# Kernel tuning notes

Hardware: AMD Instinct MI355X
Metric: run time of the kernel (lower is better)

## Reference

```python
import jax, jax.numpy as jnp
import numpy as np
from jax import lax

DIM = 256
MOTION = 128
HEADS = 8
HID = int(DIM * 3.0)
EPS = 1e-5


def std_ln(x, w, b):
    # standard nn.LayerNorm: biased var, /sqrt(var+eps)
    mean = x.mean(-1, keepdims=True)
    var = jnp.var(x, axis=-1, keepdims=True)
    return w * (x - mean) / jnp.sqrt(var + EPS) + b


def custom_ln(x, w, b):
    # repo's custom LayerNorm: UNBIASED std (ddof=1) and divide by (std+eps)
    mean = x.mean(-1, keepdims=True)
    std = jnp.std(x, axis=-1, ddof=1, keepdims=True)
    return w * (x - mean) / (std + EPS) + b


def setup_inputs() -> dict:
    key = jax.random.key(0)
    ks = jax.random.split(key, 32)
    s = 0.02
    d = {}
    d['x'] = jax.random.normal(ks[0], (4, 16384, DIM), jnp.float32)
    d['cor'] = jax.random.uniform(ks[1], (4, 128, 128, 2), jnp.float32)
    # attention projections (qkv_bias=False)
    d['q_w'] = jax.random.normal(ks[2], (DIM, DIM), jnp.float32) * s
    d['kv_w'] = jax.random.normal(ks[3], (2 * DIM, DIM), jnp.float32) * s
    d['cor_w'] = jax.random.normal(ks[4], (MOTION, 2), jnp.float32) * s
    hd = DIM // HEADS
    md = MOTION // HEADS
    d['kln_w'] = jnp.ones((HEADS, 1, hd), jnp.float32)
    d['kln_b'] = jnp.zeros((HEADS, 1, hd), jnp.float32)
    d['vln_w'] = jnp.ones((HEADS, 1, hd), jnp.float32)
    d['vln_b'] = jnp.zeros((HEADS, 1, hd), jnp.float32)
    d['corln_w'] = jnp.ones((HEADS, 1, md), jnp.float32)
    d['corln_b'] = jnp.zeros((HEADS, 1, md), jnp.float32)
    d['op1_w'] = jax.random.normal(ks[5], (DIM, DIM), jnp.float32) * s
    d['op1_b'] = jnp.zeros((DIM,), jnp.float32)
    d['op2_w'] = jax.random.normal(ks[6], (DIM, DIM), jnp.float32) * s
    d['op2_b'] = jnp.zeros((DIM,), jnp.float32)
    d['om1_w'] = jax.random.normal(ks[7], (MOTION, MOTION), jnp.float32) * s
    d['om1_b'] = jnp.zeros((MOTION,), jnp.float32)
    d['om2_w'] = jax.random.normal(ks[8], (MOTION, MOTION), jnp.float32) * s
    d['om2_b'] = jnp.zeros((MOTION,), jnp.float32)
    d['norm1_w'] = jnp.ones((DIM,), jnp.float32)
    d['norm1_b'] = jnp.zeros((DIM,), jnp.float32)
    d['norm2_w'] = jnp.ones((DIM,), jnp.float32)
    d['norm2_b'] = jnp.zeros((DIM,), jnp.float32)
    d['fc1_w'] = jax.random.normal(ks[9], (HID, DIM), jnp.float32) * s
    d['fc1_b'] = jnp.zeros((HID,), jnp.float32)
    d['dw_w'] = jax.random.normal(ks[10], (HID, 1, 3, 3), jnp.float32) * np.sqrt(2.0 / 9.0)
    d['dw_b'] = jnp.zeros((HID,), jnp.float32)
    d['fc2_w'] = jax.random.normal(ks[11], (DIM, HID), jnp.float32) * s
    d['fc2_b'] = jnp.zeros((DIM,), jnp.float32)
    d['H'] = 128
    d['W'] = 128
    d['B'] = 2
    return d


def _forward(x, cor, q_w, kv_w, cor_w, kln_w, kln_b, vln_w, vln_b,
             corln_w, corln_b, op1_w, op1_b, op2_w, op2_b,
             om1_w, om1_b, om2_w, om2_b, norm1_w, norm1_b,
             norm2_w, norm2_b, fc1_w, fc1_b, dw_w, dw_b, fc2_w, fc2_b,
             H, W, B):
    gelu = lambda t: jax.nn.gelu(t, approximate=False)
    nwB = 2 * B
    N = H * W
    C = x.shape[-1]
    M = cor_w.shape[0]
    h = kln_w.shape[0]
    hd = C // h
    md = M // h
    hid = fc1_w.shape[0]

    xw = x.reshape(nwB, N, C)            # window_partition with full window == identity
    corw = cor.reshape(nwB, N, 2)

    xn = std_ln(xw, norm1_w, norm1_b)
    half = nwB // 2
    xr = jnp.concatenate([xn[half:], xn[:half]], axis=0)  # swap frame halves

    q = (xn @ q_w.T).reshape(nwB, N, h, hd).transpose(0, 2, 1, 3)          # bhnd
    kv = (xr @ kv_w.T).reshape(nwB, N, 2, h, hd)
    k = kv[:, :, 0].transpose(0, 2, 1, 3)
    v = kv[:, :, 1].transpose(0, 2, 1, 3)
    ce_flat = corw @ cor_w.T                                               # (nwB,N,M)
    ce = ce_flat.reshape(nwB, N, h, md).transpose(0, 2, 1, 3)

    k = custom_ln(k, kln_w, kln_b)
    v = custom_ln(v, vln_w, vln_b)
    ce = custom_ln(ce, corln_w, corln_b)

    # linear attention: (k^T v)/N then q @ .
    ktv = jnp.einsum('bhnd,bhne->bhde', k, v) / N
    app = jnp.einsum('bhnd,bhde->bhne', q, ktv).transpose(0, 2, 1, 3).reshape(nwB, N, C)
    t = app + xn                                   # shortcut bias = x_norm
    x_app = gelu(t @ op1_w.T + op1_b) @ op2_w.T + op2_b + xn

    ktc = jnp.einsum('bhnd,bhne->bhde', k, ce) / N
    crev = jnp.einsum('bhnd,bhde->bhne', q, ktc).transpose(0, 2, 1, 3).reshape(nwB, N, M)
    dm = crev - ce_flat
    motion = gelu(dm @ om1_w.T + om1_b) @ om2_w.T + om2_b

    x_back = xn + x_app

    # Mlp with depthwise conv
    y = std_ln(x_back, norm2_w, norm2_b)
    h1 = y @ fc1_w.T + fc1_b                       # (nwB,N,hid)
    img = h1.transpose(0, 2, 1).reshape(nwB, hid, H, W)
    conv = lax.conv_general_dilated(img, dw_w, (1, 1), 'SAME',
                                    feature_group_count=hid,
                                    dimension_numbers=('NCHW', 'OIHW', 'NCHW'))
    conv = conv + dw_b[None, :, None, None]
    h2 = gelu(conv.reshape(nwB, hid, N).transpose(0, 2, 1))
    out = h2 @ fc2_w.T + fc2_b

    x_out = xw + out
    return x_out, motion


def reference(x, cor, q_w, kv_w, cor_w, kln_w, kln_b, vln_w, vln_b,
              corln_w, corln_b, op1_w, op1_b, op2_w, op2_b,
              om1_w, om1_b, om2_w, om2_b, norm1_w, norm1_b,
              norm2_w, norm2_b, fc1_w, fc1_b, dw_w, dw_b, fc2_w, fc2_b,
              H, W, B):
    return _forward(x, cor, q_w, kv_w, cor_w, kln_w, kln_b, vln_w, vln_b,
                    corln_w, corln_b, op1_w, op1_b, op2_w, op2_b,
                    om1_w, om1_b, om2_w, om2_b, norm1_w, norm1_b,
                    norm2_w, norm2_b, fc1_w, fc1_b, dw_w, dw_b, fc2_w, fc2_b,
                    H, W, B)
```

## Files before the change

kernel.cpp:

```cpp
#include <hip/hip_runtime.h>
#include <hip/hip_bf16.h>

#define NTOK 65536

typedef __attribute__((ext_vector_type(4))) float f32x4;
typedef __attribute__((ext_vector_type(8))) short bf16x8;

__device__ __forceinline__ float gelu_f(float x){
    float z = -2.30234438f * fmaf(0.044715f * x * x, x, x);
    float e = exp2f(z);
    return x * __builtin_amdgcn_rcpf(1.0f + e);
}
__device__ __forceinline__ float bf2f(unsigned short u){
    union { unsigned int i; float f; } w; w.i = ((unsigned int)u) << 16; return w.f;
}
__device__ __forceinline__ unsigned short f2bf(float f){
    __hip_bfloat16 h = __float2bfloat16(f);
    return *reinterpret_cast<unsigned short*>(&h);
}

__global__ __launch_bounds__(256) void wconv_kernel(const float* __restrict__ q_w, const float* __restrict__ kv_w,
                                                    const float* __restrict__ op1_w, const float* __restrict__ op2_w,
                                                    const float* __restrict__ om1_w, const float* __restrict__ om2_w,
                                                    const float* __restrict__ fc1_w, const float* __restrict__ fc2_w,
                                                    unsigned short* __restrict__ Wb){
    size_t e = ((size_t)blockIdx.x * 256 + threadIdx.x) * 4;
    if (e >= 753664) return;
    const float* src; size_t off;
    if      (e <  65536){ src = q_w;   off = 0; }
    else if (e < 196608){ src = kv_w;  off = 65536; }
    else if (e < 262144){ src = op1_w; off = 196608; }
    else if (e < 327680){ src = op2_w; off = 262144; }
    else if (e < 344064){ src = om1_w; off = 327680; }
    else if (e < 360448){ src = om2_w; off = 344064; }
    else if (e < 557056){ src = fc1_w; off = 360448; }
    else                { src = fc2_w; off = 557056; }
    float4 v = *reinterpret_cast<const float4*>(src + (e - off));
    ushort4 o; o.x = f2bf(v.x); o.y = f2bf(v.y); o.z = f2bf(v.z); o.w = f2bf(v.w);
    *reinterpret_cast<ushort4*>(Wb + e) = o;
}

template<bool BF16IN>
__global__ __launch_bounds__(256) void stdln_kernel(const void* __restrict__ Xp,
                                                    const float* __restrict__ w,
                                                    const float* __restrict__ b,
                                                    unsigned short* __restrict__ out){
    int wv = threadIdx.x >> 6, lane = threadIdx.x & 63;
    int tok0 = (blockIdx.x * 4 + wv) * 8;
    int c0 = lane * 4;
    float4 w4 = *reinterpret_cast<const float4*>(w + c0);
    float4 b4 = *reinterpret_cast<const float4*>(b + c0);
    #pragma unroll 2
    for (int j = 0; j < 8; j++){
        size_t base = (size_t)(tok0 + j) * 256 + c0;
        float v[4];
        if constexpr (BF16IN){
            ushort4 u = *reinterpret_cast<const ushort4*>((const unsigned short*)Xp + base);
            v[0] = bf2f(u.x); v[1] = bf2f(u.y); v[2] = bf2f(u.z); v[3] = bf2f(u.w);
        } else {
            float4 f = *reinterpret_cast<const float4*>((const float*)Xp + base);
            v[0] = f.x; v[1] = f.y; v[2] = f.z; v[3] = f.w;
        }
        float s = v[0] + v[1] + v[2] + v[3];
        #pragma unroll
        for (int m = 1; m < 64; m <<= 1) s += __shfl_xor(s, m, 64);
        float mean = s * (1.0f / 256.0f);
        float ss = 0;
        #pragma unroll
        for (int k = 0; k < 4; k++){ v[k] -= mean; ss = fmaf(v[k], v[k], ss); }
        #pragma unroll
        for (int m = 1; m < 64; m <<= 1) ss += __shfl_xor(ss, m, 64);
        float inv = rsqrtf(ss * (1.0f / 256.0f) + 1e-5f);
        ushort4 o;
        o.x = f2bf(w4.x * v[0] * inv + b4.x);
        o.y = f2bf(w4.y * v[1] * inv + b4.y);
        o.z = f2bf(w4.z * v[2] * inv + b4.z);
        o.w = f2bf(w4.w * v[3] * inv + b4.w);
        *reinterpret_cast<ushort4*>(out + base) = o;
    }
}

__global__ __launch_bounds__(256) void ce_kernel(const float* __restrict__ cor,
                                                 const float* __restrict__ cor_w,
                                                 unsigned short* __restrict__ CEF){
    int m = threadIdx.x & 127, half = threadIdx.x >> 7;
    float w0 = cor_w[m * 2 + 0], w1 = cor_w[m * 2 + 1];
    #pragma unroll 4
    for (int it = 0; it < 16; it++){
        int tok = blockIdx.x * 32 + it * 2 + half;
        float c0 = cor[(size_t)tok * 2 + 0];
        float c1 = cor[(size_t)tok * 2 + 1];
        CEF[(size_t)tok * 128 + m] = f2bf(c0 * w0 + c1 * w1);
    }
}

__global__ __launch_bounds__(256) void ktvc_kernel(const unsigned short* __restrict__ Kb,
                                                   const unsigned short* __restrict__ Vb,
                                                   const unsigned short* __restrict__ CEF,
                                                   const float* __restrict__ kw, const float* __restrict__ kbb,
                                                   const float* __restrict__ vw, const float* __restrict__ vbb,
                                                   const float* __restrict__ cw, const float* __restrict__ cbb,
                                                   float* __restrict__ KTV, float* __restrict__ KTC){
    int bh = blockIdx.x, b = bh >> 3, h = bh & 7;
    __shared__ float Ks[64][33];
    __shared__ float Vs[64][33];
    __shared__ float Cs[64][17];
    int t = threadIdx.x;
    int lr = t >> 2, lq = t & 3;
    int d0 = (t >> 4) * 2, e0 = (t & 15) * 2, e1 = t & 15;
    float kwr[8], kbr[8], vwr[8], vbr[8], cwr[4], cbr[4];
    #pragma unroll
    for (int j = 0; j < 8; j++){
        kwr[j] = kw[h * 32 + lq * 8 + j]; kbr[j] = kbb[h * 32 + lq * 8 + j];
        vwr[j] = vw[h * 32 + lq * 8 + j]; vbr[j] = vbb[h * 32 + lq * 8 + j];
    }
    #pragma unroll
    for (int j = 0; j < 4; j++){
        cwr[j] = cw[h * 16 + lq * 4 + j]; cbr[j] = cbb[h * 16 + lq * 4 + j];
    }
    float a00 = 0, a01 = 0, a10 = 0, a11 = 0;
    float c0a = 0, c1a = 0;
    size_t base = ((size_t)b << 14) + (size_t)blockIdx.y * 1024;
    for (int n0 = 0; n0 < 1024; n0 += 64){
        size_t rowi = base + n0 + lr;
        const ushort4* kp = reinterpret_cast<const ushort4*>(Kb + rowi * 256 + h * 32 + lq * 8);
        ushort4 ka = kp[0], kc = kp[1];
        const ushort4* vp = reinterpret_cast<const ushort4*>(Vb + rowi * 256 + h * 32 + lq * 8);
        ushort4 va = vp[0], vc = vp[1];
        ushort4 ca = *reinterpret_cast<const ushort4*>(CEF + rowi * 128 + h * 16 + lq * 4);
        float kvv[8] = { bf2f(ka.x), bf2f(ka.y), bf2f(ka.z), bf2f(ka.w),
                         bf2f(kc.x), bf2f(kc.y), bf2f(kc.z), bf2f(kc.w) };
        float vvv[8] = { bf2f(va.x), bf2f(va.y), bf2f(va.z), bf2f(va.w),
                         bf2f(vc.x), bf2f(vc.y), bf2f(vc.z), bf2f(vc.w) };
        float cvv[4] = { bf2f(ca.x), bf2f(ca.y), bf2f(ca.z), bf2f(ca.w) };
        float s = 0;
        #pragma unroll
        for (int j = 0; j < 8; j++) s += kvv[j];
        s += __shfl_xor(s, 1, 64); s += __shfl_xor(s, 2, 64);
        float mean = s * (1.0f / 32.0f);
        float ss = 0;
        #pragma unroll
        for (int j = 0; j < 8; j++){ kvv[j] -= mean; ss = fmaf(kvv[j], kvv[j], ss); }
        ss += __shfl_xor(ss, 1, 64); ss += __shfl_xor(ss, 2, 64);
        float inv = 1.0f / (sqrtf(ss * (1.0f / 31.0f)) + 1e-5f);
        #pragma unroll
        for (int j = 0; j < 8; j++) kvv[j] = fmaf(kwr[j] * kvv[j], inv, kbr[j]);
        s = 0;
        #pragma unroll
        for (int j = 0; j < 8; j++) s += vvv[j];
        s += __shfl_xor(s, 1, 64); s += __shfl_xor(s, 2, 64);
        mean = s * (1.0f / 32.0f);
        ss = 0;
        #pragma unroll
        for (int j = 0; j < 8; j++){ vvv[j] -= mean; ss = fmaf(vvv[j], vvv[j], ss); }
        ss += __shfl_xor(ss, 1, 64); ss += __shfl_xor(ss, 2, 64);
        inv = 1.0f / (sqrtf(ss * (1.0f / 31.0f)) + 1e-5f);
        #pragma unroll
        for (int j = 0; j < 8; j++) vvv[j] = fmaf(vwr[j] * vvv[j], inv, vbr[j]);
        s = 0;
        #pragma unroll
        for (int j = 0; j < 4; j++) s += cvv[j];
        s += __shfl_xor(s, 1, 64); s += __shfl_xor(s, 2, 64);
        mean = s * (1.0f / 16.0f);
        ss = 0;
        #pragma unroll
        for (int j = 0; j < 4; j++){ cvv[j] -= mean; ss = fmaf(cvv[j], cvv[j], ss); }
        ss += __shfl_xor(ss, 1, 64); ss += __shfl_xor(ss, 2, 64);
        inv = 1.0f / (sqrtf(ss * (1.0f / 15.0f)) + 1e-5f);
        #pragma unroll
        for (int j = 0; j < 4; j++) cvv[j] = fmaf(cwr[j] * cvv[j], inv, cbr[j]);
        __syncthreads();
        #pragma unroll
        for (int j = 0; j < 8; j++){ Ks[lr][lq * 8 + j] = kvv[j]; Vs[lr][lq * 8 + j] = vvv[j]; }
        #pragma unroll
        for (int j = 0; j < 4; j++) Cs[lr][lq * 4 + j] = cvv[j];
        __syncthreads();
        #pragma unroll 4
        for (int n = 0; n < 64; n++){
            float k0 = Ks[n][d0], k1 = Ks[n][d0 + 1];
            float v0 = Vs[n][e0], v1 = Vs[n][e0 + 1];
            float ce = Cs[n][e1];
            a00 = fmaf(k0, v0, a00); a01 = fmaf(k0, v1, a01);
            a10 = fmaf(k1, v0, a10); a11 = fmaf(k1, v1, a11);
            c0a = fmaf(k0, ce, c0a); c1a = fmaf(k1, ce, c1a);
        }
    }
    const float sc = 1.0f / 16384.0f;
    float* o = KTV + (size_t)bh * 1024;
    atomicAdd(&o[(d0 + 0) * 32 + e0 + 0], a00 * sc);
    atomicAdd(&o[(d0 + 0) * 32 + e0 + 1], a01 * sc);
    atomicAdd(&o[(d0 + 1) * 32 + e0 + 0], a10 * sc);
    atomicAdd(&o[(d0 + 1) * 32 + e0 + 1], a11 * sc);
    float* o2 = KTC + (size_t)bh * 512;
    atomicAdd(&o2[(d0 + 0) * 16 + e1], c0a * sc);
    atomicAdd(&o2[(d0 + 1) * 16 + e1], c1a * sc);
}

__global__ __launch_bounds__(256) void wcomb_kernel(const float* __restrict__ q_w,
                                                    const float* __restrict__ KTV,
                                                    const float* __restrict__ KTC,
                                                    unsigned short* __restrict__ WTC){
    int c = blockIdx.x;
    int b = blockIdx.y;
    int i = threadIdx.x;
    __shared__ float coef[32];
    int h = (c < 256) ? (c >> 5) : ((c - 256) >> 4);
    if (i < 32){
        if (c < 256) coef[i] = KTV[(size_t)((b * 8 + h) << 10) + i * 32 + (c & 31)];
        else         coef[i] = KTC[(size_t)((b * 8 + h) << 9)  + i * 16 + ((c - 256) & 15)];
    }
    __syncthreads();
    float acc = 0;
    #pragma unroll
    for (int d = 0; d < 32; d++) acc = fmaf(q_w[(size_t)(h * 32 + d) * 256 + i], coef[d], acc);
    WTC[((size_t)b * 384 + c) * 256 + i] = f2bf(acc);
}

__global__ __launch_bounds__(192) void dwconv_kernel(const unsigned short* __restrict__ H1,
                                                     const float* __restrict__ dww,
                                                     const float* __restrict__ dwb,
                                                     unsigned short* __restrict__ H2){
    int blk = blockIdx.x;
    int xq = blk & 3;
    int yb = (blk >> 2) & 31;
    int bb = blk >> 7;
    int y0 = yb * 4, x0 = xq * 32;
    int ch = threadIdx.x * 4;
    float w[9][4];
    #pragma unroll
    for (int k = 0; k < 9; k++)
        #pragma unroll
        for (int j = 0; j < 4; j++) w[k][j] = dww[(ch + j) * 9 + k];
    float bias[4] = { dwb[ch], dwb[ch+1], dwb[ch+2], dwb[ch+3] };
    size_t rb[6]; bool rv[6];
    #pragma unroll
    for (int r = 0; r < 6; r++){
        int yr = y0 - 1 + r;
        rv[r] = ((unsigned)yr <= 127u);
        int yc = yr < 0 ? 0 : (yr > 127 ? 127 : yr);
        rb[r] = ((size_t)((bb << 14) + (yc << 7))) * 768 + ch;
    }
    size_t ob[4];
    #pragma unroll
    for (int j = 0; j < 4; j++) ob[j] = ((size_t)((bb << 14) + ((y0 + j) << 7))) * 768 + ch;

    ushort4 cA[6], cB[6], cC[6], cD[6];
    const ushort4 Z = {0, 0, 0, 0};
    #define LOADR(DST, XX) do {                                               \
        int _x = (XX);                                                        \
        bool xv = ((unsigned)_x <= 127u);                                     \
        _Pragma("unroll")                                                     \
        for (int r = 0; r < 6; r++)                                           \
            DST[r] = (xv && rv[r]) ? *reinterpret_cast<const ushort4*>(H1 + rb[r] + (size_t)_x * 768) : Z; \
    } while (0)

    #define EMITB(SA, SB, SC, XX) do {                                        \
        _Pragma("unroll")                                                     \
        for (int j = 0; j < 4; j++){                                          \
            float acc[4];                                                     \
            _Pragma("unroll")                                                 \
            for (int q = 0; q < 4; q++) acc[q] = bias[q];                     \
            _Pragma("unroll")                                                 \
            for (int rr2 = 0; rr2 < 3; rr2++){                                \
                int ri = j + rr2;                                             \
                float a0=bf2f(SA[ri].x),a1=bf2f(SA[ri].y),a2=bf2f(SA[ri].z),a3=bf2f(SA[ri].w); \
                float b0=bf2f(SB[ri].x),b1=bf2f(SB[ri].y),b2=bf2f(SB[ri].z),b3=bf2f(SB[ri].w); \
                float c0=bf2f(SC[ri].x),c1=bf2f(SC[ri].y),c2=bf2f(SC[ri].z),c3=bf2f(SC[ri].w); \
                acc[0]=fmaf(a0,w[rr2*3+0][0],acc[0]); acc[0]=fmaf(b0,w[rr2*3+1][0],acc[0]); acc[0]=fmaf(c0,w[rr2*3+2][0],acc[0]); \
                acc[1]=fmaf(a1,w[rr2*3+0][1],acc[1]); acc[1]=fmaf(b1,w[rr2*3+1][1],acc[1]); acc[1]=fmaf(c1,w[rr2*3+2][1],acc[1]); \
                acc[2]=fmaf(a2,w[rr2*3+0][2],acc[2]); acc[2]=fmaf(b2,w[rr2*3+1][2],acc[2]); acc[2]=fmaf(c2,w[rr2*3+2][2],acc[2]); \
                acc[3]=fmaf(a3,w[rr2*3+0][3],acc[3]); acc[3]=fmaf(b3,w[rr2*3+1][3],acc[3]); acc[3]=fmaf(c3,w[rr2*3+2][3],acc[3]); \
            }                                                                 \
            ushort4 o;                                                        \
            o.x = f2bf(gelu_f(acc[0])); o.y = f2bf(gelu_f(acc[1]));           \
            o.z = f2bf(gelu_f(acc[2])); o.w = f2bf(gelu_f(acc[3]));           \
            *reinterpret_cast<ushort4*>(H2 + ob[j] + (size_t)(XX) * 768) = o; \
        }                                                                     \
    } while (0)

    LOADR(cD, x0 - 1);
    LOADR(cA, x0);
    LOADR(cB, x0 + 1);
    LOADR(cC, x0 + 2);
    #pragma unroll 1
    for (int g = 0; g < 8; g++){
        int x = x0 + g * 4;
        EMITB(cD, cA, cB, x);     LOADR(cD, x + 3);
        EMITB(cA, cB, cC, x + 1); LOADR(cA, x + 4);
        EMITB(cB, cC, cD, x + 2); LOADR(cB, x + 5);
        EMITB(cC, cD, cA, x + 3); LOADR(cC, x + 6);
    }
    #undef LOADR
    #undef EMITB
}

#define M_KV        1
#define M_BIAS_GELU 2
#define M_BIAS_ADD2 3
#define M_BIAS      4
#define M_BIAS_BF16 5
#define M_BIAS_ADDX 6
#define M_ATTN      7

template<int MODE, bool SWAP, int K, int O, int WN>
__global__ __launch_bounds__(128 * WN) void mgemm(const unsigned short* __restrict__ A,
                                                  const unsigned short* __restrict__ Wp,
                                                  const float* __restrict__ bias,
                                                  const void* __restrict__ add,
                                                  void* __restrict__ out0,
                                                  void* __restrict__ out1){
    constexpr int WAVES = 2 * WN;
    constexpr int BN = 64 * WN;
    constexpr int CH = 8 + 4 * WN;
    constexpr int NT = K / 32;
    __shared__ __align__(16) unsigned short As[2][128 * 32];
    __shared__ __align__(16) unsigned short Bs[2][BN * 32];
    const int t = threadIdx.x;
    const int lane = t & 63, wid = t >> 6;
    const int wm = wid & 1, wn = wid >> 1;
    const int row0 = blockIdx.x * 128;
    const int colB = blockIdx.y * BN;
    const unsigned short* W = Wp;
    if constexpr (MODE == M_ATTN) W += (size_t)(row0 >> 14) * (384 * 256);
    f32x4 acc[4][4];
    #pragma unroll
    for (int i = 0; i < 4; i++)
        #pragma unroll
        for (int j = 0; j < 4; j++){ f32x4 z = {0.f, 0.f, 0.f, 0.f}; acc[i][j] = z; }

    const int lr = lane >> 2;
    const int ls = lane & 3;
    const int kq = lane >> 4;
    const int rr = lane & 15;

    auto STAGE = [&](int buf, int kb){
        #pragma unroll
        for (int c = wid; c < CH; c += WAVES){
            int r16 = (c < 8) ? c : (c - 8);
            int row = r16 * 16 + lr;
            int ko = ls ^ ((row >> 1) & 3);
            if (c < 8){
                int ga = row0 + row;
                if (SWAP) ga ^= 32768;
                __builtin_amdgcn_global_load_lds(
                    (const __attribute__((address_space(1))) unsigned int*)(A + (size_t)ga * K + kb + ko * 8),
                    (__attribute__((address_space(3))) unsigned int*)(As[buf] + r16 * 512),
                    16, 0, 0);
            } else {
                int gc = colB + row;
                __builtin_amdgcn_global_load_lds(
                    (const __attribute__((address_space(1))) unsigned int*)(W + (size_t)gc * K + kb + ko * 8),
                    (__attribute__((address_space(3))) unsigned int*)(Bs[buf] + r16 * 512),
                    16, 0, 0);
            }
        }
    };

    STAGE(0, 0);
    asm volatile("s_waitcnt vmcnt(0)" ::: "memory");
    __builtin_amdgcn_s_barrier();
    #pragma unroll 1
    for (int tt = 0; tt < NT; tt++){
        int cur = tt & 1;
        if (tt + 1 < NT) STAGE(cur ^ 1, (tt + 1) * 32);
        bf16x8 af[4], bfr[4];
        #pragma unroll
        for (int m = 0; m < 4; m++){
            int row = wm * 64 + m * 16 + rr;
            int s = kq ^ ((row >> 1) & 3);
            af[m] = *reinterpret_cast<const bf16x8*>(As[cur] + row * 32 + s * 8);
        }
        #pragma unroll
        for (int n = 0; n < 4; n++){
            int row = wn * 64 + n * 16 + rr;
            int s = kq ^ ((row >> 1) & 3);
            bfr[n] = *reinterpret_cast<const bf16x8*>(Bs[cur] + row * 32 + s * 8);
        }
        #pragma unroll
        for (int m = 0; m < 4; m++)
            #pragma unroll
            for (int n = 0; n < 4; n++)
                acc[m][n] = __builtin_amdgcn_mfma_f32_16x16x32_bf16(af[m], bfr[n], acc[m][n], 0, 0, 0);
        if (tt + 1 < NT){
            asm volatile("s_waitcnt vmcnt(0)" ::: "memory");
            __builtin_amdgcn_s_barrier();
        }
    }

    #pragma unroll
    for (int m = 0; m < 4; m++){
        #pragma unroll
        for (int n = 0; n < 4; n++){
            int col = colB + wn * 64 + n * 16 + rr;
            int rbase = row0 + wm * 64 + m * 16 + kq * 4;
            #pragma unroll
            for (int j = 0; j < 4; j++){
                int r = rbase + j;
                float v = acc[m][n][j];
                size_t o = (size_t)r * O + col;
                if constexpr (MODE == M_KV){
                    if (col < 256) ((unsigned short*)out0)[(size_t)r * 256 + col] = f2bf(v);
                    else           ((unsigned short*)out1)[(size_t)r * 256 + col - 256] = f2bf(v);
                } else if constexpr (MODE == M_BIAS_GELU){
                    ((unsigned short*)out0)[o] = f2bf(gelu_f(v + bias[col]));
                } else if constexpr (MODE == M_BIAS_ADD2){
                    ((unsigned short*)out0)[o] = f2bf(v + bias[col] + 2.0f * bf2f(((const unsigned short*)add)[o]));
                } else if constexpr (MODE == M_BIAS){
                    ((float*)out0)[o] = v + bias[col];
                } else if constexpr (MODE == M_BIAS_BF16){
                    ((unsigned short*)out0)[o] = f2bf(v + bias[col]);
                } else if constexpr (MODE == M_BIAS_ADDX){
                    ((float*)out0)[o] = v + bias[col] + ((const float*)add)[o];
                } else if constexpr (MODE == M_ATTN){
                    if (col < 256){
                        size_t o1 = (size_t)r * 256 + col;
                        ((unsigned short*)out0)[o1] = f2bf(v + bf2f(((const unsigned short*)add)[o1]));
                    } else {
                        size_t o2 = (size_t)r * 128 + (col - 256);
                        ((unsigned short*)out1)[o2] = f2bf(v - bf2f(((const unsigned short*)bias)[o2]));
                    }
                }
            }
        }
    }
}

extern "C" void kernel_launch(void* const* d_in, const int* in_sizes, int n_in,
                              void* d_out, int out_size, void* d_ws, size_t ws_size,
                              hipStream_t stream){
    const float* x     = (const float*)d_in[0];
    const float* cor   = (const float*)d_in[1];
    const float* q_w   = (const float*)d_in[2];
    const float* kv_w  = (const float*)d_in[3];
    const float* cor_w = (const float*)d_in[4];
    const float* kln_w = (const float*)d_in[5];
    const float* kln_b = (const float*)d_in[6];
    const float* vln_w = (const float*)d_in[7];
    const float* vln_b = (const float*)d_in[8];
    const float* corln_w = (const float*)d_in[9];
    const float* corln_b = (const float*)d_in[10];
    const float* op1_w = (const float*)d_in[11];
    const float* op1_b = (const float*)d_in[12];
    const float* op2_w = (const float*)d_in[13];
    const float* op2_b = (const float*)d_in[14];
    const float* om1_w = (const float*)d_in[15];
    const float* om1_b = (const float*)d_in[16];
    const float* om2_w = (const float*)d_in[17];
    const float* om2_b = (const float*)d_in[18];
    const float* n1_w  = (const float*)d_in[19];
    const float* n1_b  = (const float*)d_in[20];
    const float* n2_w  = (const float*)d_in[21];
    const float* n2_b  = (const float*)d_in[22];
    const float* fc1_w = (const float*)d_in[23];
    const float* fc1_b = (const float*)d_in[24];
    const float* dw_w  = (const float*)d_in[25];
    const float* dw_b  = (const float*)d_in[26];
    const float* fc2_w = (const float*)d_in[27];
    const float* fc2_b = (const float*)d_in[28];

    unsigned short* XN  = (unsigned short*)d_ws;
    unsigned short* Qb  = XN  + (size_t)NTOK * 256;
    unsigned short* Kb  = Qb  + (size_t)NTOK * 256;
    unsigned short* Vb  = Kb  + (size_t)NTOK * 256;
    unsigned short* CEF = Vb  + (size_t)NTOK * 256;
    unsigned short* CE  = CEF + (size_t)NTOK * 128;
    float* KTV = (float*)(CE + (size_t)NTOK * 128);
    float* KTC = KTV + 32768;
    unsigned short* WTC = (unsigned short*)(KTC + 16384);
    unsigned short* Wb  = WTC + 4 * 384 * 256;
    unsigned short* H2  = Wb + 753664;
    unsigned short* T1 = Vb;
    unsigned short* T2 = Kb;
    unsigned short* XB = Qb;
    unsigned short* Y  = Vb;
    unsigned short* TM = CE;
    unsigned short* MH = CEF;
    unsigned short* H1 = XN;
    float* xout = (float*)d_out;
    float* mout = xout + (size_t)NTOK * 256;

    unsigned short* w_kv  = Wb + 65536;
    unsigned short* w_op1 = Wb + 196608;
    unsigned short* w_op2 = Wb + 262144;
    unsigned short* w_om1 = Wb + 327680;
    unsigned short* w_om2 = Wb + 344064;
    unsigned short* w_fc1 = Wb + 360448;
    unsigned short* w_fc2 = Wb + 557056;

    wconv_kernel<<<736, 256, 0, stream>>>(q_w, kv_w, op1_w, op2_w, om1_w, om2_w, fc1_w, fc2_w, Wb);
    stdln_kernel<false><<<2048, 256, 0, stream>>>(x, n1_w, n1_b, XN);
    mgemm<M_KV, true, 256, 512, 4><<<dim3(512, 2), 512, 0, stream>>>(XN, w_kv, nullptr, nullptr, Kb, Vb);
    ce_kernel<<<2048, 256, 0, stream>>>(cor, cor_w, CEF);
    hipMemsetAsync(KTV, 0, (32768 + 16384) * sizeof(float), stream);
    ktvc_kernel<<<dim3(32, 16), 256, 0, stream>>>(Kb, Vb, CEF, kln_w, kln_b, vln_w, vln_b,
                                                  corln_w, corln_b, KTV, KTC);
    wcomb_kernel<<<dim3(384, 4), 256, 0, stream>>>(q_w, KTV, KTC, WTC);
    mgemm<M_ATTN, false, 256, 384, 6><<<dim3(512, 1), 768, 0, stream>>>(XN, WTC, (const float*)CEF, XN, T1, TM);
    mgemm<M_BIAS_GELU, false, 256, 256, 4><<<dim3(512, 1), 512, 0, stream>>>(T1, w_op1, op1_b, nullptr, T2, nullptr);
    mgemm<M_BIAS_ADD2, false, 256, 256, 4><<<dim3(512, 1), 512, 0, stream>>>(T2, w_op2, op2_b, XN, XB, nullptr);
    mgemm<M_BIAS_GELU, false, 128, 128, 2><<<dim3(512, 1), 256, 0, stream>>>(TM, w_om1, om1_b, nullptr, MH, nullptr);
    mgemm<M_BIAS, false, 128, 128, 2><<<dim3(512, 1), 256, 0, stream>>>(MH, w_om2, om2_b, nullptr, mout, nullptr);
    stdln_kernel<true><<<2048, 256, 0, stream>>>(XB, n2_w, n2_b, Y);
    mgemm<M_BIAS_BF16, false, 256, 768, 6><<<dim3(512, 2), 768, 0, stream>>>(Y, w_fc1, fc1_b, nullptr, H1, nullptr);
    dwconv_kernel<<<512, 192, 0, stream>>>(H1, dw_w, dw_b, H2);
    mgemm<M_BIAS_ADDX, false, 768, 256, 4><<<dim3(512, 1), 512, 0, stream>>>(H2, w_fc2, fc2_b, x, xout, nullptr);
}
```

Baseline: 443.8 us.

## Register-tile KTV/KTC accumulation with 4x4 blocks and split tokens across warp groups

The K^T V and K^T C accumulation loop in ktvc_kernel now has each thread compute a 4x4 KV tile plus a 4x2 KC tile using vectorized float4/float2 shared-memory loads. The four wavefronts each take a quarter of every 64-token chunk, and their partial sums are combined through a shared-memory tree before the atomic adds. The grid doubles along y (512 tokens per block instead of 1024) to keep parallelism up. This is meant to cut LDS traffic per FMA and raise arithmetic intensity, at the cost of extra syncs, more shared memory and more global atomics.

```diff
diff --git a/kernel.cpp b/kernel.cpp
--- a/kernel.cpp
+++ b/kernel.cpp
@@ -102,12 +102,14 @@
                                                    const float* __restrict__ cw, const float* __restrict__ cbb,
                                                    float* __restrict__ KTV, float* __restrict__ KTC){
     int bh = blockIdx.x, b = bh >> 3, h = bh & 7;
-    __shared__ float Ks[64][33];
-    __shared__ float Vs[64][33];
-    __shared__ float Cs[64][17];
+    __shared__ float Ks[64][36];
+    __shared__ float Vs[64][36];
+    __shared__ float Cs[64][20];
+    __shared__ float P[2][64][24];
     int t = threadIdx.x;
     int lr = t >> 2, lq = t & 3;
-    int d0 = (t >> 4) * 2, e0 = (t & 15) * 2, e1 = t & 15;
+    int g = t >> 6, tl = t & 63;
+    int d0 = (tl >> 3) * 4, e0 = (tl & 7) * 4, e0c = (tl & 7) * 2;
     float kwr[8], kbr[8], vwr[8], vbr[8], cwr[4], cbr[4];
     #pragma unroll
     for (int j = 0; j < 8; j++){
@@ -118,10 +120,10 @@
     for (int j = 0; j < 4; j++){
         cwr[j] = cw[h * 16 + lq * 4 + j]; cbr[j] = cbb[h * 16 + lq * 4 + j];
     }
-    float a00 = 0, a01 = 0, a10 = 0, a11 = 0;
-    float c0a = 0, c1a = 0;
-    size_t base = ((size_t)b << 14) + (size_t)blockIdx.y * 1024;
-    for (int n0 = 0; n0 < 1024; n0 += 64){
+    float akv[4][4] = {};
+    float akc[4][2] = {};
+    size_t base = ((size_t)b << 14) + (size_t)blockIdx.y * 512;
+    for (int n0 = 0; n0 < 512; n0 += 64){
         size_t rowi = base + n0 + lr;
         const ushort4* kp = reinterpret_cast<const ushort4*>(Kb + rowi * 256 + h * 32 + lq * 8);
         ushort4 ka = kp[0], kc = kp[1];
@@ -176,24 +178,72 @@
         for (int j = 0; j < 4; j++) Cs[lr][lq * 4 + j] = cvv[j];
         __syncthreads();
         #pragma unroll 4
-        for (int n = 0; n < 64; n++){
-            float k0 = Ks[n][d0], k1 = Ks[n][d0 + 1];
-            float v0 = Vs[n][e0], v1 = Vs[n][e0 + 1];
-            float ce = Cs[n][e1];
-            a00 = fmaf(k0, v0, a00); a01 = fmaf(k0, v1, a01);
-            a10 = fmaf(k1, v0, a10); a11 = fmaf(k1, v1, a11);
-            c0a = fmaf(k0, ce, c0a); c1a = fmaf(k1, ce, c1a);
-        }
-    }
-    const float sc = 1.0f / 16384.0f;
-    float* o = KTV + (size_t)bh * 1024;
-    atomicAdd(&o[(d0 + 0) * 32 + e0 + 0], a00 * sc);
-    atomicAdd(&o[(d0 + 0) * 32 + e0 + 1], a01 * sc);
-    atomicAdd(&o[(d0 + 1) * 32 + e0 + 0], a10 * sc);
-    atomicAdd(&o[(d0 + 1) * 32 + e0 + 1], a11 * sc);
-    float* o2 = KTC + (size_t)bh * 512;
-    atomicAdd(&o2[(d0 + 0) * 16 + e1], c0a * sc);
-    atomicAdd(&o2[(d0 + 1) * 16 + e1], c1a * sc);
+        for (int i = 0; i < 16; i++){
+            int n = g * 16 + i;
+            float4 k4 = *reinterpret_cast<const float4*>(&Ks[n][d0]);
+            float4 v4 = *reinterpret_cast<const float4*>(&Vs[n][e0]);
+            float2 c2 = *reinterpret_cast<const float2*>(&Cs[n][e0c]);
+            float kk[4] = { k4.x, k4.y, k4.z, k4.w };
+            float vv[4] = { v4.x, v4.y, v4.z, v4.w };
+            #pragma unroll
+            for (int a = 0; a < 4; a++){
+                akv[a][0] = fmaf(kk[a], vv[0], akv[a][0]);
+                akv[a][1] = fmaf(kk[a], vv[1], akv[a][1]);
+                akv[a][2] = fmaf(kk[a], vv[2], akv[a][2]);
+                akv[a][3] = fmaf(kk[a], vv[3], akv[a][3]);
+                akc[a][0] = fmaf(kk[a], c2.x, akc[a][0]);
+                akc[a][1] = fmaf(kk[a], c2.y, akc[a][1]);
+            }
+        }
+    }
+    __syncthreads();
+    if (g >= 2){
+        float* p = &P[g - 2][tl][0];
+        #pragma unroll
+        for (int a = 0; a < 4; a++){
+            #pragma unroll
+            for (int e = 0; e < 4; e++) p[a * 4 + e] = akv[a][e];
+            p[16 + a * 2 + 0] = akc[a][0];
+            p[16 + a * 2 + 1] = akc[a][1];
+        }
+    }
+    __syncthreads();
+    if (g < 2){
+        const float* p = &P[g][tl][0];
+        #pragma unroll
+        for (int a = 0; a < 4; a++){
+            #pragma unroll
+            for (int e = 0; e < 4; e++) akv[a][e] += p[a * 4 + e];
+            akc[a][0] += p[16 + a * 2 + 0];
+            akc[a][1] += p[16 + a * 2 + 1];
+        }
+    }
+    __syncthreads();
+    if (g == 1){
+        float* p = &P[0][tl][0];
+        #pragma unroll
+        for (int a = 0; a < 4; a++){
+            #pragma unroll
+            for (int e = 0; e < 4; e++) p[a * 4 + e] = akv[a][e];
+            p[16 + a * 2 + 0] = akc[a][0];
+            p[16 + a * 2 + 1] = akc[a][1];
+        }
+    }
+    __syncthreads();
+    if (g == 0){
+        const float* p = &P[0][tl][0];
+        const float sc = 1.0f / 16384.0f;
+        float* o = KTV + (size_t)bh * 1024;
+        float* o2 = KTC + (size_t)bh * 512;
+        #pragma unroll
+        for (int a = 0; a < 4; a++){
+            #pragma unroll
+            for (int e = 0; e < 4; e++)
+                atomicAdd(&o[(d0 + a) * 32 + e0 + e], (akv[a][e] + p[a * 4 + e]) * sc);
+            atomicAdd(&o2[(d0 + a) * 16 + e0c + 0], (akc[a][0] + p[16 + a * 2 + 0]) * sc);
+            atomicAdd(&o2[(d0 + a) * 16 + e0c + 1], (akc[a][1] + p[16 + a * 2 + 1]) * sc);
+        }
+    }
 }
 
 __global__ __launch_bounds__(256) void wcomb_kernel(const float* __restrict__ q_w,
@@ -492,7 +542,7 @@
     mgemm<M_KV, true, 256, 512, 4><<<dim3(512, 2), 512, 0, stream>>>(XN, w_kv, nullptr, nullptr, Kb, Vb);
     ce_kernel<<<2048, 256, 0, stream>>>(cor, cor_w, CEF);
     hipMemsetAsync(KTV, 0, (32768 + 16384) * sizeof(float), stream);
-    ktvc_kernel<<<dim3(32, 16), 256, 0, stream>>>(Kb, Vb, CEF, kln_w, kln_b, vln_w, vln_b,
+    ktvc_kernel<<<dim3(32, 32), 256, 0, stream>>>(Kb, Vb, CEF, kln_w, kln_b, vln_w, vln_b,
                                                   corln_w, corln_b, KTV, KTC);
     wcomb_kernel<<<dim3(384, 4), 256, 0, stream>>>(q_w, KTV, KTC, WTC);
     mgemm<M_ATTN, false, 256, 384, 6><<<dim3(512, 1), 768, 0, stream>>>(XN, WTC, (const float*)CEF, XN, T1, TM);
```

New measurement: 424.2 us. 1.05x faster.
